# Kernel optimization log

Hardware: AMD Instinct MI355X
Metric: run time of the kernel (lower is better)

Reference implementation:

```python
import jax, jax.numpy as jnp
import numpy as np
from jax import lax

D_MODEL, D_INNER, D_CONV, DT_RANK, D_STATE, SEQ_LEN = 1024, 2048, 4, 64, 16, 4096


def setup_inputs() -> dict:
    key = jax.random.key(0)
    ks = jax.random.split(key, 9)
    s = 0.02
    x = jax.random.normal(ks[0], (SEQ_LEN, D_MODEL), dtype=jnp.float32)
    W_in = jax.random.normal(ks[1], (2 * D_INNER, D_MODEL), dtype=jnp.float32) * s
    conv_w = jax.random.normal(ks[2], (D_INNER, 1, D_CONV), dtype=jnp.float32) * 0.2  # depthwise (O,I/g,K)
    conv_b = jax.random.normal(ks[3], (D_INNER,), dtype=jnp.float32) * s
    W_x = jax.random.normal(ks[4], (DT_RANK + 2 * D_STATE, D_INNER), dtype=jnp.float32) * s
    W_dt = jax.random.normal(ks[5], (D_INNER, DT_RANK), dtype=jnp.float32) * s
    b_dt = jax.random.normal(ks[6], (D_INNER,), dtype=jnp.float32) * s
    # canonical S4D-real init: A[d, n] = n+1 -> A_log = log(1..d_state), tiled over d_inner
    A_log = jnp.log(jnp.tile(jnp.arange(1, D_STATE + 1, dtype=jnp.float32), (D_INNER, 1)))
    D = jnp.ones((D_INNER,), dtype=jnp.float32)
    W_out = jax.random.normal(ks[7], (D_MODEL, D_INNER), dtype=jnp.float32) * s
    return {"x": x, "W_in": W_in, "conv_w": conv_w, "conv_b": conv_b,
            "W_x": W_x, "W_dt": W_dt, "b_dt": b_dt, "A_log": A_log, "D": D,
            "W_out": W_out}


def _causal_depthwise_conv(x_ld, conv_w, conv_b):
    # x_ld: (L, d_inner). eqx Conv1d with padding=d_conv-1 then [:, :L] == left-pad causal conv.
    k = conv_w.shape[-1]
    xp = jnp.pad(x_ld, ((k - 1, 0), (0, 0)))  # (L+k-1, d)
    lhs = xp.T[None]  # (1, d, L+k-1)
    out = lax.conv_general_dilated(
        lhs, conv_w, window_strides=(1,), padding='VALID',
        dimension_numbers=('NCH', 'OIH', 'NCH'),
        feature_group_count=x_ld.shape[1])  # (1, d, L)
    return (out[0] + conv_b[:, None]).T  # (L, d)


def reference(x, W_in, conv_w, conv_b, W_x, W_dt, b_dt, A_log, D, W_out):
    L = x.shape[0]
    d_inner, d_state = A_log.shape
    dt_rank = W_dt.shape[1]

    xr = x @ W_in.T                      # (L, 2*d_inner)
    xi, res = jnp.split(xr, 2, axis=-1)  # each (L, d_inner)
    xs = jax.nn.silu(_causal_depthwise_conv(xi, conv_w, conv_b))  # (L, d_inner)

    # selective SSM
    dbl = xs @ W_x.T                     # (L, dt_rank + 2*d_state)
    dt_in, B, C = jnp.split(dbl, [dt_rank, dt_rank + d_state], axis=-1)
    delta = jax.nn.softplus(dt_in @ W_dt.T + b_dt)       # (L, d_inner)
    A = -jnp.exp(A_log)                                  # (d_inner, d_state)
    dA = jnp.exp(delta[:, :, None] * A[None])            # (L, d, n)
    dBu = delta[:, :, None] * B[:, None, :] * xs[:, :, None]  # (L, d, n)

    def step(h, ab):
        a, b = ab
        h = a * h + b
        return h, h

    _, hs = lax.scan(step, jnp.zeros((d_inner, d_state), dtype=x.dtype), (dA, dBu))
    y = jnp.einsum('ldn,ln->ld', hs, C) + xs * D         # (L, d_inner)

    y = y * jax.nn.silu(res)
    return y @ W_out.T                                   # (L, d_model)
```

## Files before the change

kernel.cpp:

```cpp
#include <hip/hip_runtime.h>
#include <cstdint>
#include <cstddef>

#define LSEQ 4096
#define DM 1024
#define DI 2048
#define DCONV 4
#define DRNK 64
#define DSTATE 16
#define DXW 96
#define NCH 64
#define CLEN 64
#define KSPLIT 8

typedef unsigned short ushort_t;
typedef __bf16 bfx8 __attribute__((ext_vector_type(8)));
typedef float  fx4  __attribute__((ext_vector_type(4)));
typedef float  fx16 __attribute__((ext_vector_type(16)));
typedef ushort_t usx8 __attribute__((ext_vector_type(8)));

__device__ __forceinline__ float siluf(float x) { return x / (1.f + __expf(-x)); }
__device__ __forceinline__ float softplusf(float x) {
  return fmaxf(x, 0.f) + log1pf(__expf(-fabsf(x)));
}
__device__ __forceinline__ ushort_t f2b(float x) {
  __bf16 b = (__bf16)x;
  return __builtin_bit_cast(ushort_t, b);
}
__device__ __forceinline__ float b2f(ushort_t u) {
  unsigned int x = ((unsigned int)u) << 16;
  return __builtin_bit_cast(float, x);
}
__device__ __forceinline__ void async16(const void* g, void* l) {
  __builtin_amdgcn_global_load_lds(
      (const __attribute__((address_space(1))) unsigned int*)g,
      (__attribute__((address_space(3))) unsigned int*)l, 16, 0, 0);
}

__global__ __launch_bounds__(512) void gemm_wide(
    const ushort_t* __restrict__ A, int lda,
    const ushort_t* __restrict__ B, int ldb,
    ushort_t* __restrict__ C, int ldc, int K)
{
  __shared__ ushort_t As[256 * 64];
  __shared__ ushort_t Bs[128 * 64];
  const int tid  = threadIdx.x;
  const int m0   = blockIdx.y * 256, n0 = blockIdx.x * 128;
  const int lane = tid & 63;
  const int wave = tid >> 6;
  const int wm   = (wave >> 1) * 64;
  const int wn   = (wave & 1) * 64;
  const int lm   = lane & 31;
  const int kg   = lane >> 5;
  const int r0  = tid >> 3;
  const int pos = tid & 7;
  const int cswz = (pos ^ (r0 & 7)) * 8;
  const int key  = lm & 7;

  fx16 acc[2][2] = {};

  const ushort_t* ga = A + (size_t)(m0 + r0) * lda + cswz;
  const ushort_t* gb = B + (size_t)(n0 + r0) * ldb + cswz;

  for (int k0 = 0; k0 < K; k0 += 64) {
#pragma unroll
    for (int t = 0; t < 4; ++t)
      async16(ga + (size_t)(64 * t) * lda + k0, &As[t * 64 * 64 + tid * 8]);
#pragma unroll
    for (int t = 0; t < 2; ++t)
      async16(gb + (size_t)(64 * t) * ldb + k0, &Bs[t * 64 * 64 + tid * 8]);
    __syncthreads();

#pragma unroll
    for (int kk = 0; kk < 4; ++kk) {
      const int swz = ((kk * 2 + kg) ^ key) * 8;
      bfx8 af[2], bfr[2];
#pragma unroll
      for (int i = 0; i < 2; ++i)
        af[i] = *(const bfx8*)&As[(wm + i * 32 + lm) * 64 + swz];
#pragma unroll
      for (int j = 0; j < 2; ++j)
        bfr[j] = *(const bfx8*)&Bs[(wn + j * 32 + lm) * 64 + swz];
#pragma unroll
      for (int i = 0; i < 2; ++i)
#pragma unroll
        for (int j = 0; j < 2; ++j)
          acc[i][j] = __builtin_amdgcn_mfma_f32_32x32x16_bf16(af[i], bfr[j], acc[i][j], 0, 0, 0);
    }
    __syncthreads();
  }

#pragma unroll
  for (int i = 0; i < 2; ++i)
#pragma unroll
    for (int j = 0; j < 2; ++j)
#pragma unroll
      for (int r = 0; r < 16; ++r) {
        const int lrow = (r & 3) + 8 * (r >> 2) + 4 * kg;
        C[(size_t)(m0 + wm + i * 32 + lrow) * ldc + n0 + wn + j * 32 + lm] =
            f2b(acc[i][j][r]);
      }
}

template <int EPI, int BN>
__global__ __launch_bounds__(256) void gemm32(
    const ushort_t* __restrict__ A, int lda,
    const ushort_t* __restrict__ B, int ldb,
    void* __restrict__ Cv, int ldc, int K)
{
  constexpr int MI = 2;
  constexpr int NJ = BN / 64;
  __shared__ ushort_t As[128 * 64];
  __shared__ ushort_t Bs[BN * 64];
  const int tid  = threadIdx.x;
  const int m0   = blockIdx.y * 128, n0 = blockIdx.x * BN;
  const int lane = tid & 63;
  const int wave = tid >> 6;
  const int wm   = (wave >> 1) * 64, wn = (wave & 1) * (BN / 2);
  const int lm   = lane & 31;
  const int kg   = lane >> 5;
  const int r0  = tid >> 3;
  const int pos = tid & 7;
  const int cswz = (pos ^ (r0 & 7)) * 8;
  const int key  = lm & 7;

  fx16 acc[MI][NJ] = {};

  const ushort_t* ga = A + (size_t)(m0 + r0) * lda + cswz;
  const ushort_t* gb = B + (size_t)(n0 + r0) * ldb + cswz;

  for (int k0 = 0; k0 < K; k0 += 64) {
#pragma unroll
    for (int t = 0; t < 4; ++t)
      async16(ga + (size_t)(32 * t) * lda + k0, &As[t * 32 * 64 + tid * 8]);
#pragma unroll
    for (int t = 0; t < BN / 32; ++t)
      async16(gb + (size_t)(32 * t) * ldb + k0, &Bs[t * 32 * 64 + tid * 8]);
    __syncthreads();

#pragma unroll
    for (int kk = 0; kk < 4; ++kk) {
      const int swz = ((kk * 2 + kg) ^ key) * 8;
      bfx8 af[MI], bfr[NJ];
#pragma unroll
      for (int i = 0; i < MI; ++i)
        af[i] = *(const bfx8*)&As[(wm + i * 32 + lm) * 64 + swz];
#pragma unroll
      for (int j = 0; j < NJ; ++j)
        bfr[j] = *(const bfx8*)&Bs[(wn + j * 32 + lm) * 64 + swz];
#pragma unroll
      for (int i = 0; i < MI; ++i)
#pragma unroll
        for (int j = 0; j < NJ; ++j)
          acc[i][j] = __builtin_amdgcn_mfma_f32_32x32x16_bf16(af[i], bfr[j], acc[i][j], 0, 0, 0);
    }
    __syncthreads();
  }

#pragma unroll
  for (int i = 0; i < MI; ++i)
#pragma unroll
    for (int j = 0; j < NJ; ++j)
#pragma unroll
      for (int r = 0; r < 16; ++r) {
        const int lrow = (r & 3) + 8 * (r >> 2) + 4 * kg;
        const size_t rowoff =
            (size_t)(m0 + wm + i * 32 + lrow) * ldc + n0 + wn + j * 32 + lm;
        if (EPI == 1) ((ushort_t*)Cv)[rowoff] = f2b(acc[i][j][r]);
        else          ((float*)Cv)[rowoff]   = acc[i][j][r];
      }
}

__global__ __launch_bounds__(256) void gemm_delta(
    const ushort_t* __restrict__ A,
    const ushort_t* __restrict__ B,
    const float* __restrict__ bias,
    ushort_t* __restrict__ C)
{
  __shared__ ushort_t As[128 * 64];
  __shared__ ushort_t Bs[128 * 64];
  const int tid  = threadIdx.x;
  const int m0   = blockIdx.y * 128, n0 = blockIdx.x * 128;
  const int lane = tid & 63;
  const int wave = tid >> 6;
  const int wm   = (wave >> 1) * 64, wn = (wave & 1) * 64;
  const int lm   = lane & 31;
  const int kg   = lane >> 5;
  const int r0  = tid >> 3;
  const int pos = tid & 7;
  const int cswz = (pos ^ (r0 & 7)) * 8;
  const int key  = lm & 7;

  fx16 acc[2][2] = {};

#pragma unroll
  for (int t = 0; t < 4; ++t)
    async16(A + (size_t)(m0 + r0 + 32 * t) * DRNK + cswz, &As[t * 32 * 64 + tid * 8]);
#pragma unroll
  for (int t = 0; t < 4; ++t)
    async16(B + (size_t)(n0 + r0 + 32 * t) * DRNK + cswz, &Bs[t * 32 * 64 + tid * 8]);
  __syncthreads();

#pragma unroll
  for (int kk = 0; kk < 4; ++kk) {
    const int swz = ((kk * 2 + kg) ^ key) * 8;
    bfx8 af[2], bfr[2];
#pragma unroll
    for (int i = 0; i < 2; ++i)
      af[i] = *(const bfx8*)&As[(wm + i * 32 + lm) * 64 + swz];
#pragma unroll
    for (int j = 0; j < 2; ++j)
      bfr[j] = *(const bfx8*)&Bs[(wn + j * 32 + lm) * 64 + swz];
#pragma unroll
    for (int i = 0; i < 2; ++i)
#pragma unroll
      for (int j = 0; j < 2; ++j)
        acc[i][j] = __builtin_amdgcn_mfma_f32_32x32x16_bf16(af[i], bfr[j], acc[i][j], 0, 0, 0);
  }

#pragma unroll
  for (int i = 0; i < 2; ++i)
#pragma unroll
    for (int j = 0; j < 2; ++j) {
      const int col = n0 + wn + j * 32 + lm;
      const float bv = bias[col];
#pragma unroll
      for (int r = 0; r < 16; ++r) {
        const int lrow = (r & 3) + 8 * (r >> 2) + 4 * kg;
        C[(size_t)(m0 + wm + i * 32 + lrow) * DI + col] =
            f2b(softplusf(acc[i][j][r] + bv));
      }
    }
}

__global__ __launch_bounds__(256) void gemm_dbl(
    const ushort_t* __restrict__ A, const ushort_t* __restrict__ B,
    float* __restrict__ P)
{
  __shared__ ushort_t As[128 * 64];
  __shared__ ushort_t Bs[96 * 64];
  const int tid  = threadIdx.x;
  const int m0   = blockIdx.y * 128;
  const int lane = tid & 63;
  const int wave = tid >> 6;
  const int wm   = wave * 32;
  const int lm   = lane & 31;
  const int kg   = lane >> 5;
  const int r0  = tid >> 3;
  const int pos = tid & 7;
  const int cswz = (pos ^ (r0 & 7)) * 8;
  const int key  = lm & 7;
  const int kbeg = blockIdx.z * (DI / KSPLIT);

  fx16 acc[3] = {};

  const ushort_t* ga = A + (size_t)(m0 + r0) * DI + kbeg + cswz;
  const ushort_t* gb = B + (size_t)r0 * DI + kbeg + cswz;

  for (int k0 = 0; k0 < DI / KSPLIT; k0 += 64) {
#pragma unroll
    for (int t = 0; t < 4; ++t)
      async16(ga + (size_t)(32 * t) * DI + k0, &As[t * 32 * 64 + tid * 8]);
#pragma unroll
    for (int t = 0; t < 3; ++t)
      async16(gb + (size_t)(32 * t) * DI + k0, &Bs[t * 32 * 64 + tid * 8]);
    __syncthreads();

#pragma unroll
    for (int kk = 0; kk < 4; ++kk) {
      const int swz = ((kk * 2 + kg) ^ key) * 8;
      bfx8 af = *(const bfx8*)&As[(wm + lm) * 64 + swz];
      bfx8 bfr[3];
#pragma unroll
      for (int j = 0; j < 3; ++j)
        bfr[j] = *(const bfx8*)&Bs[(j * 32 + lm) * 64 + swz];
#pragma unroll
      for (int j = 0; j < 3; ++j)
        acc[j] = __builtin_amdgcn_mfma_f32_32x32x16_bf16(af, bfr[j], acc[j], 0, 0, 0);
    }
    __syncthreads();
  }

  float* base = P + (size_t)blockIdx.z * LSEQ * DXW;
#pragma unroll
  for (int j = 0; j < 3; ++j)
#pragma unroll
    for (int r = 0; r < 16; ++r) {
      const int lrow = (r & 3) + 8 * (r >> 2) + 4 * kg;
      base[(size_t)(m0 + wm + lrow) * DXW + j * 32 + lm] = acc[j][r];
    }
}

__global__ __launch_bounds__(256) void reduce_dbl(
    const float* __restrict__ P, ushort_t* __restrict__ dtb,
    float* __restrict__ dblBC)
{
  const int f = blockIdx.x * 256 + threadIdx.x;
  float s = 0.f;
#pragma unroll
  for (int z = 0; z < KSPLIT; ++z) s += P[(size_t)z * LSEQ * DXW + f];
  const int l = f / DXW;
  const int c = f - l * DXW;
  if (c < DRNK) dtb[(size_t)l * DRNK + c] = f2b(s);
  else          dblBC[(size_t)l * 32 + (c - DRNK)] = s;
}

#define CSZ0 (LSEQ * DM)
#define CSZ1 (2 * DI * DM)
#define CSZ2 (DM * DI)
#define CSZ3 (DXW * DI)
#define CSZ4 (DI * DRNK)
#define CTOT (CSZ0 + CSZ1 + CSZ2 + CSZ3 + CSZ4)

__global__ __launch_bounds__(256) void cast_all(
    const float* __restrict__ x, const float* __restrict__ W_in,
    const float* __restrict__ W_out, const float* __restrict__ W_x,
    const float* __restrict__ W_dt,
    ushort_t* __restrict__ xb, ushort_t* __restrict__ W_inb,
    ushort_t* __restrict__ W_outb, ushort_t* __restrict__ W_xb,
    ushort_t* __restrict__ W_dtb)
{
  int i = (blockIdx.x * 256 + threadIdx.x) * 4;
  if (i >= CTOT) return;
  const float* src; ushort_t* dst;
  if (i < CSZ0) { src = x + i; dst = xb + i; }
  else if (i < CSZ0 + CSZ1) { int o = i - CSZ0; src = W_in + o; dst = W_inb + o; }
  else if (i < CSZ0 + CSZ1 + CSZ2) { int o = i - CSZ0 - CSZ1; src = W_out + o; dst = W_outb + o; }
  else if (i < CSZ0 + CSZ1 + CSZ2 + CSZ3) { int o = i - CSZ0 - CSZ1 - CSZ2; src = W_x + o; dst = W_xb + o; }
  else { int o = i - CSZ0 - CSZ1 - CSZ2 - CSZ3; src = W_dt + o; dst = W_dtb + o; }
  float4 v = *(const float4*)src;
  ushort4 o4;
  o4.x = f2b(v.x); o4.y = f2b(v.y); o4.z = f2b(v.z); o4.w = f2b(v.w);
  *(ushort4*)dst = o4;
}

__global__ __launch_bounds__(256) void conv2(
    const ushort_t* __restrict__ xrb, const float* __restrict__ cw,
    const float* __restrict__ cb, ushort_t* __restrict__ xsb)
{
  const int d0 = threadIdx.x * 8;
  const int l0 = blockIdx.x * 8;

  float4 w[8];
#pragma unroll
  for (int j = 0; j < 8; ++j) w[j] = *(const float4*)(cw + (size_t)(d0 + j) * DCONV);
  float cbv[8];
  *(float4*)&cbv[0] = *(const float4*)(cb + d0);
  *(float4*)&cbv[4] = *(const float4*)(cb + d0 + 4);

  float h0[8], h1[8], h2[8];
#pragma unroll
  for (int j = 0; j < 8; ++j) { h0[j] = 0.f; h1[j] = 0.f; h2[j] = 0.f; }
  if (l0 >= 3) {
    usx8 u0 = *(const usx8*)(xrb + (size_t)(l0 - 3) * (2 * DI) + d0);
    usx8 u1 = *(const usx8*)(xrb + (size_t)(l0 - 2) * (2 * DI) + d0);
    usx8 u2 = *(const usx8*)(xrb + (size_t)(l0 - 1) * (2 * DI) + d0);
#pragma unroll
    for (int j = 0; j < 8; ++j) { h0[j] = b2f(u0[j]); h1[j] = b2f(u1[j]); h2[j] = b2f(u2[j]); }
  }

#pragma unroll
  for (int i = 0; i < 8; ++i) {
    const int l = l0 + i;
    usx8 uc = *(const usx8*)(xrb + (size_t)l * (2 * DI) + d0);
    float c[8];
#pragma unroll
    for (int j = 0; j < 8; ++j) c[j] = b2f(uc[j]);
    usx8 o;
#pragma unroll
    for (int j = 0; j < 8; ++j) {
      float acc = cbv[j];
      acc = fmaf(w[j].x, h0[j], acc);
      acc = fmaf(w[j].y, h1[j], acc);
      acc = fmaf(w[j].z, h2[j], acc);
      acc = fmaf(w[j].w, c[j], acc);
      o[j] = f2b(siluf(acc));
    }
    *(usx8*)(xsb + (size_t)l * DI + d0) = o;
#pragma unroll
    for (int j = 0; j < 8; ++j) { h0[j] = h1[j]; h1[j] = h2[j]; h2[j] = c[j]; }
  }
}

__device__ __forceinline__ bool chain_ok(const float* Av) {
  bool ok = true;
#pragma unroll
  for (int n = 0; n < DSTATE; ++n)
    ok = ok && (fabsf(Av[n] + (float)(n + 1)) < 1e-4f);
  return ok;
}

__global__ __launch_bounds__(256) void scan_pass1(
    const ushort_t* __restrict__ deltab, const ushort_t* __restrict__ xsb,
    const float* __restrict__ dblBC, const float* __restrict__ A_log,
    float* __restrict__ sd, float* __restrict__ cS)
{
  const int tid = threadIdx.x;
  const int g = blockIdx.x;
  const int c = blockIdx.y;
  const int d = g * 256 + tid;
  __shared__ ushort_t Dsh[CLEN * 256];
  __shared__ ushort_t Ush[CLEN * 256];
  __shared__ float Bsh[CLEN][DSTATE];

  const size_t rowbase = (size_t)(c * CLEN) * DI + g * 256;
  for (int i = tid; i < CLEN * 32; i += 256) {
    const int l = i >> 5;
    const int o = (i & 31) * 8;
    *(usx8*)&Dsh[l * 256 + o] = *(const usx8*)(deltab + rowbase + (size_t)l * DI + o);
    *(usx8*)&Ush[l * 256 + o] = *(const usx8*)(xsb   + rowbase + (size_t)l * DI + o);
  }
  for (int i = tid; i < CLEN * DSTATE; i += 256) {
    const int l = i >> 4, n = i & 15;
    Bsh[l][n] = dblBC[(size_t)(c * CLEN + l) * 32 + n];
  }
  __syncthreads();

  float Av[DSTATE], h[DSTATE];
#pragma unroll
  for (int n = 0; n < DSTATE; ++n) {
    Av[n] = -__expf(A_log[d * DSTATE + n]);
    h[n] = 0.f;
  }
  const size_t base = (size_t)c * DI * DSTATE + (size_t)d * DSTATE;
  float sdv = 0.f;

  if (chain_ok(Av)) {
    for (int l = 0; l < CLEN; ++l) {
      const float dlt = b2f(Dsh[l * 256 + tid]);
      const float du = dlt * b2f(Ush[l * 256 + tid]);
      sdv += dlt;
      const float q = __expf(-dlt);
      float dAn = 1.f;
#pragma unroll
      for (int n = 0; n < DSTATE; ++n) {
        dAn *= q;
        h[n] = fmaf(dAn, h[n], du * Bsh[l][n]);
      }
    }
  } else {
    for (int l = 0; l < CLEN; ++l) {
      const float dlt = b2f(Dsh[l * 256 + tid]);
      const float du = dlt * b2f(Ush[l * 256 + tid]);
      sdv += dlt;
#pragma unroll
      for (int n = 0; n < DSTATE; ++n) {
        const float dA = __expf(dlt * Av[n]);
        h[n] = fmaf(dA, h[n], du * Bsh[l][n]);
      }
    }
  }
  sd[(size_t)c * DI + d] = sdv;
#pragma unroll
  for (int n = 0; n < DSTATE; ++n) cS[base + n] = h[n];
}

__global__ __launch_bounds__(64) void scan_pass2(
    const float* __restrict__ sd, const float* __restrict__ cS,
    const float* __restrict__ A_log, float* __restrict__ ch0)
{
  const int dn = blockIdx.x * 64 + threadIdx.x;
  const int d = dn >> 4;
  const float av = -__expf(A_log[dn]);
  float h = 0.f;
  for (int c = 0; c < NCH; ++c) {
    const size_t o = (size_t)c * DI * DSTATE + dn;
    const float s = cS[o];
    const float p = __expf(av * sd[(size_t)c * DI + d]);
    ch0[o] = h;
    h = fmaf(p, h, s);
  }
}

__global__ __launch_bounds__(256) void scan_pass3(
    const ushort_t* __restrict__ deltab, const ushort_t* __restrict__ xsb,
    const float* __restrict__ dblBC, const float* __restrict__ A_log,
    const float* __restrict__ ch0, const float* __restrict__ Dp,
    const ushort_t* __restrict__ xrb, ushort_t* __restrict__ y1b)
{
  const int tid = threadIdx.x;
  const int g = blockIdx.x;
  const int c = blockIdx.y;
  const int d = g * 256 + tid;
  __shared__ ushort_t Dsh[CLEN * 256];
  __shared__ ushort_t Ush[CLEN * 256];
  __shared__ float Bsh[CLEN][DSTATE];
  __shared__ float Csh[CLEN][DSTATE];

  const size_t rowbase = (size_t)(c * CLEN) * DI + g * 256;
  for (int i = tid; i < CLEN * 32; i += 256) {
    const int l = i >> 5;
    const int o = (i & 31) * 8;
    *(usx8*)&Dsh[l * 256 + o] = *(const usx8*)(deltab + rowbase + (size_t)l * DI + o);
    *(usx8*)&Ush[l * 256 + o] = *(const usx8*)(xsb   + rowbase + (size_t)l * DI + o);
  }
  for (int i = tid; i < CLEN * DSTATE; i += 256) {
    const int l = i >> 4, n = i & 15;
    const size_t row = (size_t)(c * CLEN + l) * 32;
    Bsh[l][n] = dblBC[row + n];
    Csh[l][n] = dblBC[row + 16 + n];
  }
  __syncthreads();

  float Av[DSTATE], h[DSTATE];
  const size_t base = (size_t)c * DI * DSTATE + (size_t)d * DSTATE;
#pragma unroll
  for (int n = 0; n < DSTATE; ++n) {
    Av[n] = -__expf(A_log[d * DSTATE + n]);
    h[n] = ch0[base + n];
  }
  const float Dd = Dp[d];
  const ushort_t* resp = xrb + (size_t)(c * CLEN) * (2 * DI) + DI + d;
  ushort_t* yp = y1b + (size_t)(c * CLEN) * DI + d;

  if (chain_ok(Av)) {
    for (int l = 0; l < CLEN; ++l) {
      const float dlt = b2f(Dsh[l * 256 + tid]);
      const float u = b2f(Ush[l * 256 + tid]);
      const float du = dlt * u;
      const float q = __expf(-dlt);
      float dAn = 1.f;
      float y = 0.f;
#pragma unroll
      for (int n = 0; n < DSTATE; ++n) {
        dAn *= q;
        h[n] = fmaf(dAn, h[n], du * Bsh[l][n]);
        y = fmaf(h[n], Csh[l][n], y);
      }
      y = fmaf(u, Dd, y);
      const float res = b2f(resp[(size_t)l * (2 * DI)]);
      yp[(size_t)l * DI] = f2b(y * siluf(res));
    }
  } else {
    for (int l = 0; l < CLEN; ++l) {
      const float dlt = b2f(Dsh[l * 256 + tid]);
      const float u = b2f(Ush[l * 256 + tid]);
      const float du = dlt * u;
      float y = 0.f;
#pragma unroll
      for (int n = 0; n < DSTATE; ++n) {
        const float dA = __expf(dlt * Av[n]);
        h[n] = fmaf(dA, h[n], du * Bsh[l][n]);
        y = fmaf(h[n], Csh[l][n], y);
      }
      y = fmaf(u, Dd, y);
      const float res = b2f(resp[(size_t)l * (2 * DI)]);
      yp[(size_t)l * DI] = f2b(y * siluf(res));
    }
  }
}

extern "C" void kernel_launch(void* const* d_in, const int* in_sizes, int n_in,
                              void* d_out, int out_size, void* d_ws, size_t ws_size,
                              hipStream_t stream) {
  (void)in_sizes; (void)n_in; (void)out_size; (void)ws_size;
  const float* x      = (const float*)d_in[0];
  const float* W_in   = (const float*)d_in[1];
  const float* conv_w = (const float*)d_in[2];
  const float* conv_b = (const float*)d_in[3];
  const float* W_x    = (const float*)d_in[4];
  const float* W_dt   = (const float*)d_in[5];
  const float* b_dt   = (const float*)d_in[6];
  const float* A_log  = (const float*)d_in[7];
  const float* Dp     = (const float*)d_in[8];
  const float* W_out  = (const float*)d_in[9];
  float* out = (float*)d_out;

  float* ws    = (float*)d_ws;
  float* sd    = ws;
  float* cS    = sd + (size_t)NCH * DI;
  float* ch0   = cS + (size_t)NCH * DI * DSTATE;
  ushort_t* deltab = (ushort_t*)(ch0 + (size_t)NCH * DI * DSTATE);
  ushort_t* xrb   = deltab + (size_t)LSEQ * DI;
  ushort_t* xsb   = xrb   + (size_t)LSEQ * 2 * DI;
  ushort_t* y1b   = xsb   + (size_t)LSEQ * DI;
  ushort_t* xb    = y1b   + (size_t)LSEQ * DI;
  ushort_t* W_inb = xb    + (size_t)LSEQ * DM;
  ushort_t* W_outb= W_inb + (size_t)2 * DI * DM;
  ushort_t* W_xb  = W_outb+ (size_t)DM * DI;
  ushort_t* W_dtb = W_xb  + (size_t)DXW * DI;
  ushort_t* dtb   = W_dtb + (size_t)DI * DRNK;
  float* dblBC = (float*)(dtb + (size_t)LSEQ * DRNK);
  float* partial = ws;

  hipLaunchKernelGGL(cast_all, dim3((CTOT / 4 + 255) / 256), dim3(256), 0, stream,
                     x, W_in, W_out, W_x, W_dt, xb, W_inb, W_outb, W_xb, W_dtb);

  hipLaunchKernelGGL(gemm_wide, dim3((2 * DI) / 128, LSEQ / 256), dim3(512), 0, stream,
                     xb, DM, W_inb, DM, xrb, 2 * DI, DM);

  hipLaunchKernelGGL(conv2, dim3(LSEQ / 8), dim3(256), 0, stream,
                     xrb, conv_w, conv_b, xsb);

  hipLaunchKernelGGL(gemm_dbl, dim3(1, LSEQ / 128, KSPLIT), dim3(256), 0, stream,
                     xsb, W_xb, partial);
  hipLaunchKernelGGL(reduce_dbl, dim3((LSEQ * DXW) / 256), dim3(256), 0, stream,
                     partial, dtb, dblBC);

  hipLaunchKernelGGL(gemm_delta, dim3(DI / 128, LSEQ / 128), dim3(256), 0, stream,
                     dtb, W_dtb, b_dt, deltab);

  hipLaunchKernelGGL(scan_pass1, dim3(DI / 256, NCH), dim3(256), 0, stream,
                     deltab, xsb, dblBC, A_log, sd, cS);
  hipLaunchKernelGGL(scan_pass2, dim3((DI * DSTATE) / 64), dim3(64), 0, stream,
                     sd, cS, A_log, ch0);
  hipLaunchKernelGGL(scan_pass3, dim3(DI / 256, NCH), dim3(256), 0, stream,
                     deltab, xsb, dblBC, A_log, ch0, Dp, xrb, y1b);

  hipLaunchKernelGGL(HIP_KERNEL_NAME(gemm32<0, 64>),
                     dim3(DM / 64, LSEQ / 128), dim3(256), 0, stream,
                     y1b, DI, W_outb, DI, (void*)out, DM, DI);
}
```

Before: 281.3 us.

## Rewrite input projection GEMM with 256x256 tiles and triple-buffered async pipeline

Replaces the input-projection GEMM with a 256x256 tile kernel. It uses a K-step of 32 and a three-stage LDS ring fed by async global-to-LDS loads issued two tiles ahead, with explicit waitcnt and barriers. It also remaps block IDs for L2 locality and raises MFMA priority with s_setprio. The goal is to hide global load latency and cut redundant operand traffic, at the cost of more registers per wave and hardcoded grid assumptions (16 column tiles, 8-way remap).

```diff
diff --git a/kernel.cpp b/kernel.cpp
--- a/kernel.cpp
+++ b/kernel.cpp
@@ -37,61 +37,103 @@
       (__attribute__((address_space(3))) unsigned int*)l, 16, 0, 0);
 }
 
-__global__ __launch_bounds__(512) void gemm_wide(
+__global__ __launch_bounds__(512) void gemm_big(
     const ushort_t* __restrict__ A, int lda,
     const ushort_t* __restrict__ B, int ldb,
     ushort_t* __restrict__ C, int ldc, int K)
 {
-  __shared__ ushort_t As[256 * 64];
-  __shared__ ushort_t Bs[128 * 64];
+  __shared__ ushort_t As[3][256 * 32];
+  __shared__ ushort_t Bs[3][256 * 32];
+
   const int tid  = threadIdx.x;
-  const int m0   = blockIdx.y * 256, n0 = blockIdx.x * 128;
+  const int lid  = blockIdx.y * gridDim.x + blockIdx.x;
+  const int sid  = (lid & 7) * 32 + (lid >> 3);
+  const int m0   = (sid >> 4) * 256;
+  const int n0   = (sid & 15) * 256;
+
   const int lane = tid & 63;
   const int wave = tid >> 6;
-  const int wm   = (wave >> 1) * 64;
-  const int wn   = (wave & 1) * 64;
+  const int wm   = (wave >> 2) * 128;
+  const int wn   = (wave & 3) * 64;
   const int lm   = lane & 31;
   const int kg   = lane >> 5;
-  const int r0  = tid >> 3;
-  const int pos = tid & 7;
-  const int cswz = (pos ^ (r0 & 7)) * 8;
-  const int key  = lm & 7;
-
-  fx16 acc[2][2] = {};
+  const int key  = (lm >> 1) & 3;
+
+  const int r0   = tid >> 2;
+  const int pos  = tid & 3;
+  const int cswz = (pos ^ ((r0 >> 1) & 3)) * 8;
+
+  fx16 acc[4][2] = {};
 
   const ushort_t* ga = A + (size_t)(m0 + r0) * lda + cswz;
   const ushort_t* gb = B + (size_t)(n0 + r0) * ldb + cswz;
 
-  for (int k0 = 0; k0 < K; k0 += 64) {
-#pragma unroll
-    for (int t = 0; t < 4; ++t)
-      async16(ga + (size_t)(64 * t) * lda + k0, &As[t * 64 * 64 + tid * 8]);
-#pragma unroll
-    for (int t = 0; t < 2; ++t)
-      async16(gb + (size_t)(64 * t) * ldb + k0, &Bs[t * 64 * 64 + tid * 8]);
-    __syncthreads();
-
-#pragma unroll
-    for (int kk = 0; kk < 4; ++kk) {
+  const int NT = K >> 5;
+
+#pragma unroll
+  for (int u = 0; u < 2; ++u) {
+#pragma unroll
+    for (int h = 0; h < 2; ++h) {
+      async16(ga + (size_t)(128 * h) * lda + u * 32, &As[u][h * 128 * 32 + tid * 8]);
+      async16(gb + (size_t)(128 * h) * ldb + u * 32, &Bs[u][h * 128 * 32 + tid * 8]);
+    }
+  }
+  asm volatile("s_waitcnt vmcnt(4)" ::: "memory");
+  __builtin_amdgcn_s_barrier();
+  __builtin_amdgcn_sched_barrier(0);
+
+  int cur = 0;
+  for (int t = 0; t < NT; ++t) {
+    const ushort_t* as = &As[cur][0];
+    const ushort_t* bs = &Bs[cur][0];
+
+    bfx8 af[2][4], bfr[2][2];
+#pragma unroll
+    for (int kk = 0; kk < 2; ++kk) {
       const int swz = ((kk * 2 + kg) ^ key) * 8;
-      bfx8 af[2], bfr[2];
-#pragma unroll
-      for (int i = 0; i < 2; ++i)
-        af[i] = *(const bfx8*)&As[(wm + i * 32 + lm) * 64 + swz];
+#pragma unroll
+      for (int i = 0; i < 4; ++i)
+        af[kk][i] = *(const bfx8*)&as[(wm + i * 32 + lm) * 32 + swz];
 #pragma unroll
       for (int j = 0; j < 2; ++j)
-        bfr[j] = *(const bfx8*)&Bs[(wn + j * 32 + lm) * 64 + swz];
-#pragma unroll
-      for (int i = 0; i < 2; ++i)
+        bfr[kk][j] = *(const bfx8*)&bs[(wn + j * 32 + lm) * 32 + swz];
+    }
+
+    if (t + 2 < NT) {
+      int s2 = cur + 2; if (s2 >= 3) s2 -= 3;
+      const int k2 = (t + 2) * 32;
+#pragma unroll
+      for (int h = 0; h < 2; ++h) {
+        async16(ga + (size_t)(128 * h) * lda + k2, &As[s2][h * 128 * 32 + tid * 8]);
+        async16(gb + (size_t)(128 * h) * ldb + k2, &Bs[s2][h * 128 * 32 + tid * 8]);
+      }
+    }
+
+    __builtin_amdgcn_s_barrier();
+    asm volatile("s_waitcnt lgkmcnt(0)" ::: "memory");
+    __builtin_amdgcn_sched_barrier(0);
+    __builtin_amdgcn_s_setprio(1);
+#pragma unroll
+    for (int kk = 0; kk < 2; ++kk)
+#pragma unroll
+      for (int i = 0; i < 4; ++i)
 #pragma unroll
         for (int j = 0; j < 2; ++j)
-          acc[i][j] = __builtin_amdgcn_mfma_f32_32x32x16_bf16(af[i], bfr[j], acc[i][j], 0, 0, 0);
-    }
-    __syncthreads();
-  }
-
-#pragma unroll
-  for (int i = 0; i < 2; ++i)
+          acc[i][j] = __builtin_amdgcn_mfma_f32_32x32x16_bf16(
+              af[kk][i], bfr[kk][j], acc[i][j], 0, 0, 0);
+    __builtin_amdgcn_s_setprio(0);
+    __builtin_amdgcn_sched_barrier(0);
+
+    if (t + 2 < NT) asm volatile("s_waitcnt vmcnt(4)" ::: "memory");
+    else            asm volatile("s_waitcnt vmcnt(0)" ::: "memory");
+    __builtin_amdgcn_s_barrier();
+    __builtin_amdgcn_sched_barrier(0);
+
+    ++cur; if (cur >= 3) cur -= 3;
+  }
+
+#pragma unroll
+  for (int i = 0; i < 4; ++i)
 #pragma unroll
     for (int j = 0; j < 2; ++j)
 #pragma unroll
@@ -586,7 +628,7 @@
   hipLaunchKernelGGL(cast_all, dim3((CTOT / 4 + 255) / 256), dim3(256), 0, stream,
                      x, W_in, W_out, W_x, W_dt, xb, W_inb, W_outb, W_xb, W_dtb);
 
-  hipLaunchKernelGGL(gemm_wide, dim3((2 * DI) / 128, LSEQ / 256), dim3(512), 0, stream,
+  hipLaunchKernelGGL(gemm_big, dim3((2 * DI) / 256, LSEQ / 256), dim3(512), 0, stream,
                      xb, DM, W_inb, DM, xrb, 2 * DI, DM);
 
   hipLaunchKernelGGL(conv2, dim3(LSEQ / 8), dim3(256), 0, stream,
```

Result: no change. 283.2 us (+0.7%).
